# Optimization experiments

Measured on AMD Instinct MI355X. Metric: run time of the kernel, lower is better.

## Reference

```python
import jax, jax.numpy as jnp
import numpy as np

SOFT_TAU = 0.5
MAX_TEMP = 40.0
LABEL_SMOOTH = 0.1


def setup_inputs() -> dict:
    key = jax.random.key(0)
    k1, k2 = jax.random.split(key)
    B, Tv, Tw, D = 64, 128, 128, 256
    video_features = jax.random.normal(k1, (B, Tv, D), dtype=jnp.float32)
    wifi_features = jax.random.normal(k2, (B, Tw, D), dtype=jnp.float32)
    logit_scale = jnp.ones((), dtype=jnp.float32)
    return {"video_features": video_features, "wifi_features": wifi_features, "logit_scale": logit_scale}


def _cross_entropy_ls(logits, labels):
    # torch CrossEntropyLoss(label_smoothing=0.1), mean reduction
    logp = jax.nn.log_softmax(logits, axis=-1)
    nll = -jnp.take_along_axis(logp, labels[:, None], axis=1)[:, 0]
    smooth = -jnp.mean(logp, axis=-1)
    return jnp.mean((1.0 - LABEL_SMOOTH) * nll + LABEL_SMOOTH * smooth)


def reference(video_features, wifi_features, logit_scale):
    B = video_features.shape[0]
    # [B, B, Tv, Tw] dense cross-modal similarity
    sim = jnp.einsum('imd,jnd->ijmn', video_features, wifi_features)
    sim_d = jax.lax.stop_gradient(sim)
    # video->wifi soft pooling over Tw
    attn_v2w = jax.nn.softmax(sim_d / SOFT_TAU, axis=3)
    soft_sim_v2w = jnp.sum(sim * attn_v2w, axis=3)  # [B, B, Tv]
    # wifi->video soft pooling over Tv
    attn_w2v = jax.nn.softmax(sim_d / SOFT_TAU, axis=2)
    soft_sim_w2v = jnp.sum(sim * attn_w2v, axis=2)  # [B, B, Tw]
    # frame-level softmax pooling to global similarity
    fw_v = jax.nn.softmax(jax.lax.stop_gradient(soft_sim_v2w) / SOFT_TAU, axis=2)
    sim_v2w_global = jnp.sum(soft_sim_v2w * fw_v, axis=2)  # [B, B]
    fw_w = jax.nn.softmax(jax.lax.stop_gradient(soft_sim_w2v) / SOFT_TAU, axis=2)
    sim_w2v_global = jnp.sum(soft_sim_w2v * fw_w, axis=2)  # [B, B]
    dense_similarity = (sim_v2w_global + sim_w2v_global) / 2.0
    scale = jnp.minimum(logit_scale, MAX_TEMP)
    logits_per_video = scale * dense_similarity
    logits_per_wifi = logits_per_video.T
    labels = jnp.arange(B, dtype=jnp.int32)
    loss_video = _cross_entropy_ls(logits_per_video, labels)
    loss_wifi = _cross_entropy_ls(logits_per_wifi, labels)
    return (loss_video + loss_wifi) / 2.0
```

## Files before the change

kernel.cpp:

```cpp
#include <hip/hip_runtime.h>
#include <hip/hip_bf16.h>

typedef __attribute__((ext_vector_type(8))) short bf16x8;
typedef __attribute__((ext_vector_type(4))) float f32x4;

#define TT 128
#define DD 256
#define BK 64
#define BPAN 16384

__device__ __forceinline__ unsigned short f2bf(float f) {
  unsigned int x = __float_as_uint(f);
  x += 0x7fffu + ((x >> 16) & 1u);
  return (unsigned short)(x >> 16);
}

__device__ __forceinline__ bf16x8 pack8(float4 lo, float4 hi) {
  bf16x8 v;
  v[0] = (short)f2bf(lo.x); v[1] = (short)f2bf(lo.y);
  v[2] = (short)f2bf(lo.z); v[3] = (short)f2bf(lo.w);
  v[4] = (short)f2bf(hi.x); v[5] = (short)f2bf(hi.y);
  v[6] = (short)f2bf(hi.z); v[7] = (short)f2bf(hi.w);
  return v;
}

__global__ __launch_bounds__(512, 4) void pair_kernel(
    const float* __restrict__ video, const float* __restrict__ wifi,
    float* __restrict__ dense) {
  __shared__ __align__(16) char lds[65536];
  const int tid = threadIdx.x;
  const int bid = blockIdx.x;
  const int bi = bid >> 6, bj = bid & 63;
  const float* __restrict__ Ag = video + (size_t)bi * (TT * DD);
  const float* __restrict__ Bg = wifi  + (size_t)bj * (TT * DD);

  const int wid = tid >> 6, l = tid & 63;
  const int l15 = l & 15;
  const int R   = (wid >> 1) * 32;
  const int Cc  = (wid & 1) * 64;
  const int xr  = (l15 & 7) << 4;
  const int lhi16 = (l >> 4) * 16;

  const int srow  = tid >> 2;
  const int scolb = (tid & 3) * 32;
  const int sswz  = (srow & 7) << 4;
  const int sb0 = srow * 128 + ((scolb)      ^ sswz);
  const int sb1 = srow * 128 + ((scolb + 16) ^ sswz);

  f32x4 acc[2][4];
#pragma unroll
  for (int m = 0; m < 2; ++m)
#pragma unroll
    for (int n = 0; n < 4; ++n) acc[m][n] = (f32x4){0.f, 0.f, 0.f, 0.f};

  const int arow0 = (R + l15) * 128;
  const int arow1 = (R + 16 + l15) * 128;
  const int brow0 = (Cc +  0 + l15) * 128 + BPAN;
  const int brow1 = (Cc + 16 + l15) * 128 + BPAN;
  const int brow2 = (Cc + 32 + l15) * 128 + BPAN;
  const int brow3 = (Cc + 48 + l15) * 128 + BPAN;

  for (int kp = 0; kp < 4; ++kp) {
    const float* pa = Ag + srow * DD + kp * BK + (tid & 3) * 16;
    const float* pb = Bg + srow * DD + kp * BK + (tid & 3) * 16;
    float4 a0 = *(const float4*)(pa);
    float4 a1 = *(const float4*)(pa + 4);
    float4 a2 = *(const float4*)(pa + 8);
    float4 a3 = *(const float4*)(pa + 12);
    float4 b0 = *(const float4*)(pb);
    float4 b1 = *(const float4*)(pb + 4);
    float4 b2 = *(const float4*)(pb + 8);
    float4 b3 = *(const float4*)(pb + 12);
    if (kp) __syncthreads();
    *(bf16x8*)(lds + sb0)        = pack8(a0, a1);
    *(bf16x8*)(lds + sb1)        = pack8(a2, a3);
    *(bf16x8*)(lds + BPAN + sb0) = pack8(b0, b1);
    *(bf16x8*)(lds + BPAN + sb1) = pack8(b2, b3);
    __syncthreads();

#pragma unroll
    for (int ks = 0; ks < 2; ++ks) {
      const int ko = (ks * 64 + lhi16) ^ xr;
      bf16x8 fa0 = *(const bf16x8*)(lds + arow0 + ko);
      bf16x8 fa1 = *(const bf16x8*)(lds + arow1 + ko);
      bf16x8 fb0 = *(const bf16x8*)(lds + brow0 + ko);
      bf16x8 fb1 = *(const bf16x8*)(lds + brow1 + ko);
      bf16x8 fb2 = *(const bf16x8*)(lds + brow2 + ko);
      bf16x8 fb3 = *(const bf16x8*)(lds + brow3 + ko);
      acc[0][0] = __builtin_amdgcn_mfma_f32_16x16x32_bf16(fa0, fb0, acc[0][0], 0, 0, 0);
      acc[0][1] = __builtin_amdgcn_mfma_f32_16x16x32_bf16(fa0, fb1, acc[0][1], 0, 0, 0);
      acc[0][2] = __builtin_amdgcn_mfma_f32_16x16x32_bf16(fa0, fb2, acc[0][2], 0, 0, 0);
      acc[0][3] = __builtin_amdgcn_mfma_f32_16x16x32_bf16(fa0, fb3, acc[0][3], 0, 0, 0);
      acc[1][0] = __builtin_amdgcn_mfma_f32_16x16x32_bf16(fa1, fb0, acc[1][0], 0, 0, 0);
      acc[1][1] = __builtin_amdgcn_mfma_f32_16x16x32_bf16(fa1, fb1, acc[1][1], 0, 0, 0);
      acc[1][2] = __builtin_amdgcn_mfma_f32_16x16x32_bf16(fa1, fb2, acc[1][2], 0, 0, 0);
      acc[1][3] = __builtin_amdgcn_mfma_f32_16x16x32_bf16(fa1, fb3, acc[1][3], 0, 0, 0);
    }
  }
  __syncthreads();

  {
    const int rbase = R + (l >> 4) * 4;
    const int cbase = Cc + l15;
#pragma unroll
    for (int m = 0; m < 2; ++m)
#pragma unroll
      for (int n = 0; n < 4; ++n)
#pragma unroll
        for (int reg = 0; reg < 4; ++reg) {
          const int row = rbase + m * 16 + reg;
          const int col = cbase + n * 16;
          *(float*)(lds + row * 512 + ((col * 4) ^ ((row & 7) << 4))) =
              acc[m][n][reg];
        }
  }
  __syncthreads();

  const int r = tid >> 2, g = tid & 3;
  float svv, sww;
  {
    float v[32];
    float mx = -3.4e38f;
    const int rswz = (r & 7) << 4;
#pragma unroll
    for (int c = 0; c < 32; ++c) {
      const int col = g + 4 * c;
      v[c] = *(const float*)(lds + r * 512 + ((col * 4) ^ rswz));
      mx = fmaxf(mx, v[c]);
    }
    mx = fmaxf(mx, __shfl_xor(mx, 1));
    mx = fmaxf(mx, __shfl_xor(mx, 2));
    float se = 0.f, sev = 0.f;
#pragma unroll
    for (int c = 0; c < 32; ++c) {
      float e = __expf((v[c] - mx) * 2.0f);
      se += e; sev += e * v[c];
    }
    se  += __shfl_xor(se, 1);  se  += __shfl_xor(se, 2);
    sev += __shfl_xor(sev, 1); sev += __shfl_xor(sev, 2);
    svv = sev / se;
  }
  {
    float v[32];
    float mx = -3.4e38f;
#pragma unroll
    for (int c = 0; c < 32; ++c) {
      const int row = g + 4 * c;
      v[c] = *(const float*)(lds + row * 512 + ((r * 4) ^ ((row & 7) << 4)));
      mx = fmaxf(mx, v[c]);
    }
    mx = fmaxf(mx, __shfl_xor(mx, 1));
    mx = fmaxf(mx, __shfl_xor(mx, 2));
    float se = 0.f, sev = 0.f;
#pragma unroll
    for (int c = 0; c < 32; ++c) {
      float e = __expf((v[c] - mx) * 2.0f);
      se += e; sev += e * v[c];
    }
    se  += __shfl_xor(se, 1);  se  += __shfl_xor(se, 2);
    sev += __shfl_xor(sev, 1); sev += __shfl_xor(sev, 2);
    sww = sev / se;
  }
  __syncthreads();
  if (g == 0) {
    *(float*)(lds + r * 4)       = svv;
    *(float*)(lds + 512 + r * 4) = sww;
  }
  __syncthreads();

  if (wid < 2) {
    const float* arr = (const float*)(lds + wid * 512);
    float a0 = arr[l], a1 = arr[l + 64];
    float mx = fmaxf(a0, a1);
#pragma unroll
    for (int s = 1; s < 64; s <<= 1) mx = fmaxf(mx, __shfl_xor(mx, s));
    float e0 = __expf((a0 - mx) * 2.0f), e1 = __expf((a1 - mx) * 2.0f);
    float se = e0 + e1, sev = e0 * a0 + e1 * a1;
#pragma unroll
    for (int s = 1; s < 64; s <<= 1) { se += __shfl_xor(se, s); sev += __shfl_xor(sev, s); }
    if (l == 0) *(float*)(lds + 1024 + wid * 4) = sev / se;
  }
  __syncthreads();
  if (tid == 0)
    dense[bid] = 0.5f * (*(const float*)(lds + 1024) + *(const float*)(lds + 1028));
}

__global__ __launch_bounds__(64) void loss_kernel(
    const float* __restrict__ dense, const float* __restrict__ scalep,
    float* __restrict__ out) {
  const int i = threadIdx.x;
  const float sc = fminf(scalep[0], 40.0f);
  float mxr = -3.4e38f, mxc = -3.4e38f;
  for (int j = 0; j < 64; ++j) {
    mxr = fmaxf(mxr, sc * dense[i * 64 + j]);
    mxc = fmaxf(mxc, sc * dense[j * 64 + i]);
  }
  float ser = 0.f, sec = 0.f, slr = 0.f, slc = 0.f;
  for (int j = 0; j < 64; ++j) {
    float zr = sc * dense[i * 64 + j];
    float zc = sc * dense[j * 64 + i];
    ser += __expf(zr - mxr); sec += __expf(zc - mxc);
    slr += zr;               slc += zc;
  }
  const float lser = mxr + logf(ser);
  const float lsec = mxc + logf(sec);
  const float zd = sc * dense[i * 65];
  float lv = lser - 0.9f * zd - 0.1f * (slr * (1.0f / 64.0f));
  float lw = lsec - 0.9f * zd - 0.1f * (slc * (1.0f / 64.0f));
  float t = 0.5f * (lv + lw);
#pragma unroll
  for (int s = 1; s < 64; s <<= 1) t += __shfl_xor(t, s);
  if (i == 0) out[0] = t * (1.0f / 64.0f);
}

extern "C" void kernel_launch(void* const* d_in, const int* in_sizes, int n_in,
                              void* d_out, int out_size, void* d_ws, size_t ws_size,
                              hipStream_t stream) {
  (void)in_sizes; (void)n_in; (void)out_size; (void)ws_size;
  const float* video = (const float*)d_in[0];
  const float* wifi  = (const float*)d_in[1];
  const float* scale = (const float*)d_in[2];
  float* dense = (float*)d_ws;

  hipLaunchKernelGGL(pair_kernel, dim3(64 * 64), dim3(512), 0, stream,
                     video, wifi, dense);
  hipLaunchKernelGGL(loss_kernel, dim3(1), dim3(64), 0, stream,
                     dense, scale, (float*)d_out);
}
```

Measured before the change: 110.7 us.

## Pre-convert inputs to bf16, double-buffer LDS loads, use 32x32 MFMA with register softmax

Adds a conversion kernel that writes bf16 copies of both inputs to workspace, so each pair block loads half the bytes through global_load_lds direct-to-LDS copies instead of converting fp32 per block. The K loop is double-buffered across two LDS stages, and the MFMA shape changes from 16x16x32 to 32x32x16 with a different warp tiling. The soft-pooling epilogue now reduces max, exp-sum and weighted sum straight from accumulator registers using partial arrays in LDS, instead of spilling the full 128x128 tile to LDS and re-reading it twice. This costs an extra kernel launch, a larger LDS footprint that may lower occupancy, and a fallback path that is taken when the workspace is too small.

```diff
diff --git a/kernel.cpp b/kernel.cpp
--- a/kernel.cpp
+++ b/kernel.cpp
@@ -2,12 +2,12 @@
 #include <hip/hip_bf16.h>
 
 typedef __attribute__((ext_vector_type(8))) short bf16x8;
-typedef __attribute__((ext_vector_type(4))) float f32x4;
+typedef __attribute__((ext_vector_type(16))) float f32x16;
+typedef __attribute__((ext_vector_type(4))) unsigned short u16x4;
 
 #define TT 128
 #define DD 256
 #define BK 64
-#define BPAN 16384
 
 __device__ __forceinline__ unsigned short f2bf(float f) {
   unsigned int x = __float_as_uint(f);
@@ -24,153 +24,167 @@
   return v;
 }
 
+__global__ __launch_bounds__(256) void conv_kernel(
+    const float* __restrict__ v, const float* __restrict__ w,
+    unsigned short* __restrict__ vb, unsigned short* __restrict__ wb) {
+  const int idx = blockIdx.x * 256 + threadIdx.x;
+  float4 a = reinterpret_cast<const float4*>(v)[idx];
+  float4 b = reinterpret_cast<const float4*>(w)[idx];
+  u16x4 pa, pb;
+  pa[0] = f2bf(a.x); pa[1] = f2bf(a.y); pa[2] = f2bf(a.z); pa[3] = f2bf(a.w);
+  pb[0] = f2bf(b.x); pb[1] = f2bf(b.y); pb[2] = f2bf(b.z); pb[3] = f2bf(b.w);
+  reinterpret_cast<u16x4*>(vb)[idx] = pa;
+  reinterpret_cast<u16x4*>(wb)[idx] = pb;
+}
+
+template <bool PRE>
 __global__ __launch_bounds__(512, 4) void pair_kernel(
-    const float* __restrict__ video, const float* __restrict__ wifi,
+    const float* __restrict__ videof, const float* __restrict__ wifif,
+    const unsigned short* __restrict__ videob,
+    const unsigned short* __restrict__ wifib,
     float* __restrict__ dense) {
-  __shared__ __align__(16) char lds[65536];
+  __shared__ __align__(16) char lds[73728];
   const int tid = threadIdx.x;
   const int bid = blockIdx.x;
   const int bi = bid >> 6, bj = bid & 63;
-  const float* __restrict__ Ag = video + (size_t)bi * (TT * DD);
-  const float* __restrict__ Bg = wifi  + (size_t)bj * (TT * DD);
-
   const int wid = tid >> 6, l = tid & 63;
-  const int l15 = l & 15;
-  const int R   = (wid >> 1) * 32;
-  const int Cc  = (wid & 1) * 64;
-  const int xr  = (l15 & 7) << 4;
-  const int lhi16 = (l >> 4) * 16;
-
-  const int srow  = tid >> 2;
-  const int scolb = (tid & 3) * 32;
-  const int sswz  = (srow & 7) << 4;
-  const int sb0 = srow * 128 + ((scolb)      ^ sswz);
-  const int sb1 = srow * 128 + ((scolb + 16) ^ sswz);
-
-  f32x4 acc[2][4];
-#pragma unroll
-  for (int m = 0; m < 2; ++m)
-#pragma unroll
-    for (int n = 0; n < 4; ++n) acc[m][n] = (f32x4){0.f, 0.f, 0.f, 0.f};
-
-  const int arow0 = (R + l15) * 128;
-  const int arow1 = (R + 16 + l15) * 128;
-  const int brow0 = (Cc +  0 + l15) * 128 + BPAN;
-  const int brow1 = (Cc + 16 + l15) * 128 + BPAN;
-  const int brow2 = (Cc + 32 + l15) * 128 + BPAN;
-  const int brow3 = (Cc + 48 + l15) * 128 + BPAN;
+  const int l31 = l & 31;
+
+  const int o  = wid >> 2;
+  const int mg = wid & 1;
+  const int cg = (wid >> 1) & 1;
+
+  const char* vsrc = (const char*)videob + (size_t)bi * (TT * DD * 2);
+  const char* wsrc = (const char*)wifib  + (size_t)bj * (TT * DD * 2);
+  const int grow8 = l >> 3;
+  const int gcb   = ((l & 7) ^ grow8) << 4;
+  const int srow = tid >> 2;
+  const int scb  = (tid & 3) * 32;
+  const int sswz = (srow & 7) << 4;
+  const int sb0  = srow * 128 + ((scb) ^ sswz);
+  const int sb1  = srow * 128 + ((scb + 16) ^ sswz);
+
+  f32x16 acc[2][2];
+#pragma unroll
+  for (int mi = 0; mi < 2; ++mi)
+#pragma unroll
+    for (int t = 0; t < 2; ++t)
+#pragma unroll
+      for (int r = 0; r < 16; ++r) acc[mi][t][r] = 0.f;
+
+  const int apan = o ? 16384 : 0;
+  const int bpan = o ? 0 : 16384;
+  const int xr   = (l & 7) << 4;
+  const int khalf = (l >> 5) * 16;
+  const int x0 = (mg * 64 + l31) * 128;
+  const int x1 = (mg * 64 + 32 + l31) * 128;
+  const int y0 = (cg * 64 + l31) * 128;
+  const int y1 = (cg * 64 + 32 + l31) * 128;
+
+#define STAGE_PRE(KP, BUF)                                                    \
+  do {                                                                        \
+    _Pragma("unroll") for (int k_ = 0; k_ < 4; ++k_) {                        \
+      const int q_ = wid * 4 + k_;                                            \
+      const int c_ = q_ & 15;                                                 \
+      const char* s_ = ((q_ < 16) ? vsrc : wsrc) + (c_ * 8 + grow8) * 512 +   \
+                       (KP) * 128 + gcb;                                      \
+      char* d_ = lds + (BUF) * 32768 + ((q_ < 16) ? 0 : 16384) + c_ * 1024;   \
+      __builtin_amdgcn_global_load_lds((const void*)s_, (void*)d_, 16, 0, 0); \
+    }                                                                         \
+  } while (0)
+
+#define STAGE_REG(KP, BUF)                                                    \
+  do {                                                                        \
+    const float* pa_ = videof + (size_t)bi * (TT * DD) + srow * DD +          \
+                       (KP) * BK + (tid & 3) * 16;                            \
+    const float* pb_ = wifif + (size_t)bj * (TT * DD) + srow * DD +           \
+                       (KP) * BK + (tid & 3) * 16;                            \
+    float4 a0_ = *(const float4*)(pa_);                                       \
+    float4 a1_ = *(const float4*)(pa_ + 4);                                   \
+    float4 a2_ = *(const float4*)(pa_ + 8);                                   \
+    float4 a3_ = *(const float4*)(pa_ + 12);                                  \
+    float4 b0_ = *(const float4*)(pb_);                                       \
+    float4 b1_ = *(const float4*)(pb_ + 4);                                   \
+    float4 b2_ = *(const float4*)(pb_ + 8);                                   \
+    float4 b3_ = *(const float4*)(pb_ + 12);                                  \
+    char* base_ = lds + (BUF) * 32768;                                        \
+    *(bf16x8*)(base_ + sb0)         = pack8(a0_, a1_);                        \
+    *(bf16x8*)(base_ + sb1)         = pack8(a2_, a3_);                        \
+    *(bf16x8*)(base_ + 16384 + sb0) = pack8(b0_, b1_);                        \
+    *(bf16x8*)(base_ + 16384 + sb1) = pack8(b2_, b3_);                        \
+  } while (0)
+
+  if constexpr (PRE) STAGE_PRE(0, 0); else STAGE_REG(0, 0);
+  __syncthreads();
 
   for (int kp = 0; kp < 4; ++kp) {
-    const float* pa = Ag + srow * DD + kp * BK + (tid & 3) * 16;
-    const float* pb = Bg + srow * DD + kp * BK + (tid & 3) * 16;
-    float4 a0 = *(const float4*)(pa);
-    float4 a1 = *(const float4*)(pa + 4);
-    float4 a2 = *(const float4*)(pa + 8);
-    float4 a3 = *(const float4*)(pa + 12);
-    float4 b0 = *(const float4*)(pb);
-    float4 b1 = *(const float4*)(pb + 4);
-    float4 b2 = *(const float4*)(pb + 8);
-    float4 b3 = *(const float4*)(pb + 12);
-    if (kp) __syncthreads();
-    *(bf16x8*)(lds + sb0)        = pack8(a0, a1);
-    *(bf16x8*)(lds + sb1)        = pack8(a2, a3);
-    *(bf16x8*)(lds + BPAN + sb0) = pack8(b0, b1);
-    *(bf16x8*)(lds + BPAN + sb1) = pack8(b2, b3);
+    const int bufoff = (kp & 1) * 32768;
+    if (kp < 3) {
+      if constexpr (PRE) STAGE_PRE(kp + 1, (kp + 1) & 1);
+      else STAGE_REG(kp + 1, (kp + 1) & 1);
+    }
+#pragma unroll
+    for (int ks = 0; ks < 4; ++ks) {
+      const int cb = ks * 32 + khalf;
+      bf16x8 ax0 = *(const bf16x8*)(lds + bufoff + apan + x0 + (cb ^ xr));
+      bf16x8 ax1 = *(const bf16x8*)(lds + bufoff + apan + x1 + (cb ^ xr));
+      bf16x8 by0 = *(const bf16x8*)(lds + bufoff + bpan + y0 + (cb ^ xr));
+      bf16x8 by1 = *(const bf16x8*)(lds + bufoff + bpan + y1 + (cb ^ xr));
+      acc[0][0] = __builtin_amdgcn_mfma_f32_32x32x16_bf16(ax0, by0, acc[0][0], 0, 0, 0);
+      acc[0][1] = __builtin_amdgcn_mfma_f32_32x32x16_bf16(ax0, by1, acc[0][1], 0, 0, 0);
+      acc[1][0] = __builtin_amdgcn_mfma_f32_32x32x16_bf16(ax1, by0, acc[1][0], 0, 0, 0);
+      acc[1][1] = __builtin_amdgcn_mfma_f32_32x32x16_bf16(ax1, by1, acc[1][1], 0, 0, 0);
+    }
     __syncthreads();
-
-#pragma unroll
-    for (int ks = 0; ks < 2; ++ks) {
-      const int ko = (ks * 64 + lhi16) ^ xr;
-      bf16x8 fa0 = *(const bf16x8*)(lds + arow0 + ko);
-      bf16x8 fa1 = *(const bf16x8*)(lds + arow1 + ko);
-      bf16x8 fb0 = *(const bf16x8*)(lds + brow0 + ko);
-      bf16x8 fb1 = *(const bf16x8*)(lds + brow1 + ko);
-      bf16x8 fb2 = *(const bf16x8*)(lds + brow2 + ko);
-      bf16x8 fb3 = *(const bf16x8*)(lds + brow3 + ko);
-      acc[0][0] = __builtin_amdgcn_mfma_f32_16x16x32_bf16(fa0, fb0, acc[0][0], 0, 0, 0);
-      acc[0][1] = __builtin_amdgcn_mfma_f32_16x16x32_bf16(fa0, fb1, acc[0][1], 0, 0, 0);
-      acc[0][2] = __builtin_amdgcn_mfma_f32_16x16x32_bf16(fa0, fb2, acc[0][2], 0, 0, 0);
-      acc[0][3] = __builtin_amdgcn_mfma_f32_16x16x32_bf16(fa0, fb3, acc[0][3], 0, 0, 0);
-      acc[1][0] = __builtin_amdgcn_mfma_f32_16x16x32_bf16(fa1, fb0, acc[1][0], 0, 0, 0);
-      acc[1][1] = __builtin_amdgcn_mfma_f32_16x16x32_bf16(fa1, fb1, acc[1][1], 0, 0, 0);
-      acc[1][2] = __builtin_amdgcn_mfma_f32_16x16x32_bf16(fa1, fb2, acc[1][2], 0, 0, 0);
-      acc[1][3] = __builtin_amdgcn_mfma_f32_16x16x32_bf16(fa1, fb3, acc[1][3], 0, 0, 0);
+  }
+
+  float* PM = (float*)(lds + 65536);
+  float* PS = PM + 512;
+  float* PV = PM + 1024;
+  float* Gb = PM + 1536;
+  const int colb = cg * 64;
+
+#pragma unroll
+  for (int t = 0; t < 2; ++t) {
+    float mx = acc[0][t][0];
+#pragma unroll
+    for (int mi = 0; mi < 2; ++mi)
+#pragma unroll
+      for (int r = 0; r < 16; ++r) mx = fmaxf(mx, acc[mi][t][r]);
+    mx = fmaxf(mx, __shfl_xor(mx, 32));
+    if (l < 32) PM[o * 256 + mg * 128 + colb + t * 32 + l] = mx;
+  }
+  __syncthreads();
+
+#pragma unroll
+  for (int t = 0; t < 2; ++t) {
+    const int c = colb + t * 32 + l31;
+    const float mx = fmaxf(PM[o * 256 + c], PM[o * 256 + 128 + c]);
+    float se = 0.f, sv = 0.f;
+#pragma unroll
+    for (int mi = 0; mi < 2; ++mi)
+#pragma unroll
+      for (int r = 0; r < 16; ++r) {
+        const float v = acc[mi][t][r];
+        const float e = __expf((v - mx) * 2.0f);
+        se += e;
+        sv = fmaf(e, v, sv);
+      }
+    se += __shfl_xor(se, 32);
+    sv += __shfl_xor(sv, 32);
+    if (l < 32) {
+      PS[o * 256 + mg * 128 + c] = se;
+      PV[o * 256 + mg * 128 + c] = sv;
     }
   }
   __syncthreads();
 
-  {
-    const int rbase = R + (l >> 4) * 4;
-    const int cbase = Cc + l15;
-#pragma unroll
-    for (int m = 0; m < 2; ++m)
-#pragma unroll
-      for (int n = 0; n < 4; ++n)
-#pragma unroll
-        for (int reg = 0; reg < 4; ++reg) {
-          const int row = rbase + m * 16 + reg;
-          const int col = cbase + n * 16;
-          *(float*)(lds + row * 512 + ((col * 4) ^ ((row & 7) << 4))) =
-              acc[m][n][reg];
-        }
-  }
-  __syncthreads();
-
-  const int r = tid >> 2, g = tid & 3;
-  float svv, sww;
-  {
-    float v[32];
-    float mx = -3.4e38f;
-    const int rswz = (r & 7) << 4;
-#pragma unroll
-    for (int c = 0; c < 32; ++c) {
-      const int col = g + 4 * c;
-      v[c] = *(const float*)(lds + r * 512 + ((col * 4) ^ rswz));
-      mx = fmaxf(mx, v[c]);
-    }
-    mx = fmaxf(mx, __shfl_xor(mx, 1));
-    mx = fmaxf(mx, __shfl_xor(mx, 2));
-    float se = 0.f, sev = 0.f;
-#pragma unroll
-    for (int c = 0; c < 32; ++c) {
-      float e = __expf((v[c] - mx) * 2.0f);
-      se += e; sev += e * v[c];
-    }
-    se  += __shfl_xor(se, 1);  se  += __shfl_xor(se, 2);
-    sev += __shfl_xor(sev, 1); sev += __shfl_xor(sev, 2);
-    svv = sev / se;
-  }
-  {
-    float v[32];
-    float mx = -3.4e38f;
-#pragma unroll
-    for (int c = 0; c < 32; ++c) {
-      const int row = g + 4 * c;
-      v[c] = *(const float*)(lds + row * 512 + ((r * 4) ^ ((row & 7) << 4)));
-      mx = fmaxf(mx, v[c]);
-    }
-    mx = fmaxf(mx, __shfl_xor(mx, 1));
-    mx = fmaxf(mx, __shfl_xor(mx, 2));
-    float se = 0.f, sev = 0.f;
-#pragma unroll
-    for (int c = 0; c < 32; ++c) {
-      float e = __expf((v[c] - mx) * 2.0f);
-      se += e; sev += e * v[c];
-    }
-    se  += __shfl_xor(se, 1);  se  += __shfl_xor(se, 2);
-    sev += __shfl_xor(sev, 1); sev += __shfl_xor(sev, 2);
-    sww = sev / se;
-  }
-  __syncthreads();
-  if (g == 0) {
-    *(float*)(lds + r * 4)       = svv;
-    *(float*)(lds + 512 + r * 4) = sww;
-  }
-  __syncthreads();
-
   if (wid < 2) {
-    const float* arr = (const float*)(lds + wid * 512);
-    float a0 = arr[l], a1 = arr[l + 64];
+    const int oo = wid == 0 ? 1 : 0;
+    const float* PSo = PS + oo * 256;
+    const float* PVo = PV + oo * 256;
+    float a0 = (PVo[l] + PVo[128 + l]) / (PSo[l] + PSo[128 + l]);
+    float a1 = (PVo[64 + l] + PVo[192 + l]) / (PSo[64 + l] + PSo[192 + l]);
     float mx = fmaxf(a0, a1);
 #pragma unroll
     for (int s = 1; s < 64; s <<= 1) mx = fmaxf(mx, __shfl_xor(mx, s));
@@ -178,11 +192,10 @@
     float se = e0 + e1, sev = e0 * a0 + e1 * a1;
 #pragma unroll
     for (int s = 1; s < 64; s <<= 1) { se += __shfl_xor(se, s); sev += __shfl_xor(sev, s); }
-    if (l == 0) *(float*)(lds + 1024 + wid * 4) = sev / se;
-  }
-  __syncthreads();
-  if (tid == 0)
-    dense[bid] = 0.5f * (*(const float*)(lds + 1024) + *(const float*)(lds + 1028));
+    if (l == 0) Gb[wid] = sev / se;
+  }
+  __syncthreads();
+  if (tid == 0) dense[bid] = 0.5f * (Gb[0] + Gb[1]);
 }
 
 __global__ __launch_bounds__(64) void loss_kernel(
@@ -216,14 +229,24 @@
 extern "C" void kernel_launch(void* const* d_in, const int* in_sizes, int n_in,
                               void* d_out, int out_size, void* d_ws, size_t ws_size,
                               hipStream_t stream) {
-  (void)in_sizes; (void)n_in; (void)out_size; (void)ws_size;
+  (void)in_sizes; (void)n_in; (void)out_size;
   const float* video = (const float*)d_in[0];
   const float* wifi  = (const float*)d_in[1];
   const float* scale = (const float*)d_in[2];
   float* dense = (float*)d_ws;
-
-  hipLaunchKernelGGL(pair_kernel, dim3(64 * 64), dim3(512), 0, stream,
-                     video, wifi, dense);
+  unsigned short* vb = (unsigned short*)((char*)d_ws + 16384);
+  unsigned short* wb = vb + 64 * TT * DD;
+
+  const bool pre = ws_size >= (size_t)16384 + 2u * 64 * TT * DD * 2;
+  if (pre) {
+    hipLaunchKernelGGL(conv_kernel, dim3(2048), dim3(256), 0, stream,
+                       video, wifi, vb, wb);
+    hipLaunchKernelGGL((pair_kernel<true>), dim3(64 * 64), dim3(512), 0, stream,
+                       video, wifi, vb, wb, dense);
+  } else {
+    hipLaunchKernelGGL((pair_kernel<false>), dim3(64 * 64), dim3(512), 0, stream,
+                       video, wifi, vb, wb, dense);
+  }
   hipLaunchKernelGGL(loss_kernel, dim3(1), dim3(64), 0, stream,
                      dense, scale, (float*)d_out);
 }
```

Measured after the change: 101.7 us. 1.09x faster.
